# Performance work log

Hardware: AMD Instinct MI355X
Metric: run time of the kernel (lower is better)

The kernel has to match this reference:

```python
import jax, jax.numpy as jnp
import numpy as np

B, T, D, K = 32, 1024, 256, 1024


def setup_inputs() -> dict:
    key = jax.random.key(0)
    k1, k2 = jax.random.split(key)
    x = jax.random.normal(k1, (B, T, D), dtype=jnp.float32)
    # nn.Embedding init: uniform(-1/emb_size, 1/emb_size)
    embedding = jax.random.uniform(k2, (K, D), dtype=jnp.float32,
                                   minval=-1.0 / K, maxval=1.0 / K)
    return {"x": x, "embedding": embedding}


def reference(x, embedding):
    # x: [B, T, D], embedding: [K, D]
    Bx, Tx, Dx = x.shape
    flat = x.reshape(-1, Dx)  # [N, D]
    dist = (jnp.sum(embedding * embedding, axis=1)
            - 2.0 * flat @ embedding.T
            + jnp.sum(flat * flat, axis=1, keepdims=True))
    quantized_idx = jnp.argmin(dist, axis=1).reshape(Bx, Tx)  # [B, T] int
    # onehot @ W  ==  gather rows of W
    embed_idx = embedding[quantized_idx]  # [B, T, D]
    # straight-through estimator
    embed_idx_qx = x + jax.lax.stop_gradient(embed_idx - x)
    return embed_idx, embed_idx_qx, quantized_idx
```

## Files before the change

### kernel.cpp

```cpp
#include <hip/hip_runtime.h>
#include <math.h>

#define N_ROWS 32768
#define DIM    256
#define KCODES 1024
#define DELTA  1.5e-4f

typedef float f32x4 __attribute__((ext_vector_type(4)));
typedef short s16x8 __attribute__((ext_vector_type(8)));

__device__ inline unsigned short bf_rne(float f) {
    unsigned u = __float_as_uint(f);
    return (unsigned short)((u + 0x7FFFu + ((u >> 16) & 1u)) >> 16);
}
__device__ inline float bf_to_f(unsigned short h) {
    return __uint_as_float(((unsigned)h) << 16);
}

__device__ inline void ins4(float v, int ix, float (&tv)[4], int (&ti)[4]) {
    if (v < tv[3] || (v == tv[3] && ix < ti[3])) {
        if (v < tv[2] || (v == tv[2] && ix < ti[2])) {
            tv[3] = tv[2]; ti[3] = ti[2];
            if (v < tv[1] || (v == tv[1] && ix < ti[1])) {
                tv[2] = tv[1]; ti[2] = ti[1];
                if (v < tv[0] || (v == tv[0] && ix < ti[0])) {
                    tv[1] = tv[0]; ti[1] = ti[0]; tv[0] = v; ti[0] = ix;
                } else { tv[1] = v; ti[1] = ix; }
            } else { tv[2] = v; ti[2] = ix; }
        } else { tv[3] = v; ti[3] = ix; }
    }
}

__device__ __forceinline__ void gl_lds16(const void* gp, void* lp) {
    __builtin_amdgcn_global_load_lds(
        (__attribute__((address_space(1))) void*)(void*)gp,
        (__attribute__((address_space(3))) void*)lp, 16, 0, 0);
}

__global__ __launch_bounds__(256) void prep_kernel(const float* __restrict__ E,
                                                   const float* __restrict__ X,
                                                   float* __restrict__ e2,
                                                   float* __restrict__ x2,
                                                   unsigned short* __restrict__ Eh,
                                                   unsigned short* __restrict__ El) {
    __shared__ float sq[4][260];
    const int wave = threadIdx.x >> 6;
    const int lane = threadIdx.x & 63;
    if (blockIdx.x < KCODES / 4) {
        const int row = blockIdx.x * 4 + wave;
        const float4* rp = (const float4*)(E + (size_t)row * DIM);
        float4 v = rp[lane];
        sq[wave][lane * 4 + 0] = v.x * v.x;
        sq[wave][lane * 4 + 1] = v.y * v.y;
        sq[wave][lane * 4 + 2] = v.z * v.z;
        sq[wave][lane * 4 + 3] = v.w * v.w;
        float fs[4] = {v.x, v.y, v.z, v.w};
        ushort4 hv, lv;
        unsigned short* hp = (unsigned short*)&hv;
        unsigned short* lp = (unsigned short*)&lv;
#pragma unroll
        for (int j = 0; j < 4; ++j) {
            unsigned short h = bf_rne(fs[j]);
            hp[j] = h;
            lp[j] = bf_rne(fs[j] - bf_to_f(h));
        }
        *(ushort4*)(Eh + (size_t)row * DIM + lane * 4) = hv;
        *(ushort4*)(El + (size_t)row * DIM + lane * 4) = lv;
        if (lane < 8) {
#pragma clang fp contract(off)
            const int j = lane;
            float rA = sq[wave][j];
#pragma unroll
            for (int m = 1; m < 16; ++m) rA += sq[wave][8 * m + j];
            float rB = sq[wave][128 + j];
#pragma unroll
            for (int m = 1; m < 16; ++m) rB += sq[wave][128 + 8 * m + j];
            rA = rA + __shfl_xor(rA, 1, 64); rA = rA + __shfl_xor(rA, 2, 64);
            rA = rA + __shfl_xor(rA, 4, 64);
            rB = rB + __shfl_xor(rB, 1, 64); rB = rB + __shfl_xor(rB, 2, 64);
            rB = rB + __shfl_xor(rB, 4, 64);
            if (j == 0) e2[row] = rA + rB;
        }
    } else {
        const int row = (blockIdx.x - KCODES / 4) * 4 + wave;
        if (row >= N_ROWS) return;
        const float4* rp = (const float4*)(X + (size_t)row * DIM);
        float4 v = rp[lane];
        sq[wave][lane * 4 + 0] = v.x * v.x;
        sq[wave][lane * 4 + 1] = v.y * v.y;
        sq[wave][lane * 4 + 2] = v.z * v.z;
        sq[wave][lane * 4 + 3] = v.w * v.w;
        if (lane < 8) {
#pragma clang fp contract(off)
            const int j = lane;
            float rA = sq[wave][j];
#pragma unroll
            for (int m = 1; m < 16; ++m) rA += sq[wave][8 * m + j];
            float rB = sq[wave][128 + j];
#pragma unroll
            for (int m = 1; m < 16; ++m) rB += sq[wave][128 + 8 * m + j];
            rA = rA + __shfl_xor(rA, 1, 64); rA = rA + __shfl_xor(rA, 2, 64);
            rA = rA + __shfl_xor(rA, 4, 64);
            rB = rB + __shfl_xor(rB, 1, 64); rB = rB + __shfl_xor(rB, 2, 64);
            rB = rB + __shfl_xor(rB, 4, 64);
            if (j == 0) x2[row] = rA + rB;
        }
    }
}

__global__ __launch_bounds__(512, 2) void vq_mfma_kernel(const float* __restrict__ X,
                                                         const unsigned short* __restrict__ Eh,
                                                         const unsigned short* __restrict__ El,
                                                         const float* __restrict__ e2g,
                                                         float* __restrict__ topv,
                                                         int* __restrict__ topi) {
    __shared__ __align__(16) short bh_lds[2][16384];
    __shared__ __align__(16) short bl_lds[2][16384];
    __shared__ float e2_lds[KCODES];

    const int tid  = threadIdx.x;
    const int w    = tid >> 6;
    const int l    = tid & 63;
    const int c16  = l & 15;
    const int quad = l >> 4;
    const int p    = w & 3;
    const int grp  = w >> 2;
    const int row0 = blockIdx.x * 128;

    if (tid < 256) *(float4*)&e2_lds[tid * 4] = *(const float4*)&e2g[tid * 4];

    s16x8 xh[2][8], xl[2][8];
#pragma unroll
    for (int t = 0; t < 2; ++t) {
        const float* xrow = X + (size_t)(row0 + p * 32 + t * 16 + c16) * DIM + quad * 8;
#pragma unroll
        for (int ks = 0; ks < 8; ++ks) {
            float4 f0 = *(const float4*)(xrow + ks * 32);
            float4 f1 = *(const float4*)(xrow + ks * 32 + 4);
            float fs[8] = {f0.x, f0.y, f0.z, f0.w, f1.x, f1.y, f1.z, f1.w};
#pragma unroll
            for (int j = 0; j < 8; ++j) {
                unsigned short h = bf_rne(fs[j]);
                xh[t][ks][j] = (short)h;
                xl[t][ks][j] = (short)bf_rne(fs[j] - bf_to_f(h));
            }
        }
    }

    float tva[4], tvb[4];
    int   tia[4], tib[4];
#pragma unroll
    for (int s = 0; s < 4; ++s) {
        tva[s] = INFINITY; tvb[s] = INFINITY;
        tia[s] = 0x7fffffff; tib[s] = 0x7fffffff;
    }

    auto stage = [&](int bsel, int cb) {
#pragma unroll
        for (int gg = 0; gg < 4; ++gg) {
            const int g  = w + gg * 8;
            const int nt = g >> 3, ks = g & 7;
            const size_t eo = (size_t)(cb + nt * 16 + c16) * DIM + ks * 32 + quad * 8;
            gl_lds16(Eh + eo, &bh_lds[bsel][g * 512]);
            gl_lds16(El + eo, &bl_lds[bsel][g * 512]);
        }
    };

    stage(0, 0);

    for (int c = 0; c < 16; ++c) {
        __syncthreads();
        if (c < 15) stage((c + 1) & 1, (c + 1) * 64);
        const int bsel = c & 1;
#pragma unroll
        for (int ntt = 0; ntt < 2; ++ntt) {
            const int nt = grp * 2 + ntt;
            f32x4 c0a = {0.f, 0.f, 0.f, 0.f};
            f32x4 c1a = c0a, c2a = c0a, c0b = c0a, c1b = c0a, c2b = c0a;
#pragma unroll
            for (int ks = 0; ks < 8; ++ks) {
                const int off = ((nt * 8 + ks) * 64 + l) * 8;
                s16x8 ch = *(const s16x8*)&bh_lds[bsel][off];
                s16x8 cl = *(const s16x8*)&bl_lds[bsel][off];
                c0a = __builtin_amdgcn_mfma_f32_16x16x32_bf16(ch, xh[0][ks], c0a, 0, 0, 0);
                c0b = __builtin_amdgcn_mfma_f32_16x16x32_bf16(ch, xh[1][ks], c0b, 0, 0, 0);
                c1a = __builtin_amdgcn_mfma_f32_16x16x32_bf16(cl, xh[0][ks], c1a, 0, 0, 0);
                c1b = __builtin_amdgcn_mfma_f32_16x16x32_bf16(cl, xh[1][ks], c1b, 0, 0, 0);
                c2a = __builtin_amdgcn_mfma_f32_16x16x32_bf16(ch, xl[0][ks], c2a, 0, 0, 0);
                c2b = __builtin_amdgcn_mfma_f32_16x16x32_bf16(ch, xl[1][ks], c2b, 0, 0, 0);
            }
#pragma unroll
            for (int r = 0; r < 4; ++r) {
                const int code = c * 64 + nt * 16 + quad * 4 + r;
                const float e2v = e2_lds[code];
                float da = c0a[r] + c1a[r] + c2a[r];
                float db = c0b[r] + c1b[r] + c2b[r];
                ins4(e2v - 2.0f * da, code, tva, tia);
                ins4(e2v - 2.0f * db, code, tvb, tib);
            }
        }
    }

#pragma unroll
    for (int st = 16; st <= 32; st <<= 1) {
        float ov[4]; int oi[4];
#pragma unroll
        for (int s = 0; s < 4; ++s) {
            ov[s] = __shfl_xor(tva[s], st, 64);
            oi[s] = __shfl_xor(tia[s], st, 64);
        }
#pragma unroll
        for (int s = 0; s < 4; ++s) ins4(ov[s], oi[s], tva, tia);
#pragma unroll
        for (int s = 0; s < 4; ++s) {
            ov[s] = __shfl_xor(tvb[s], st, 64);
            oi[s] = __shfl_xor(tib[s], st, 64);
        }
#pragma unroll
        for (int s = 0; s < 4; ++s) ins4(ov[s], oi[s], tvb, tib);
    }

    float* mv = (float*)&bh_lds[0][0];
    int*   mi = (int*)&bh_lds[0][4096];
    if (grp == 1 && quad == 0) {
        const int sa = p * 32 + c16;
        const int sb = sa + 16;
#pragma unroll
        for (int s = 0; s < 4; ++s) {
            mv[sa * 4 + s] = tva[s]; mi[sa * 4 + s] = tia[s];
            mv[sb * 4 + s] = tvb[s]; mi[sb * 4 + s] = tib[s];
        }
    }
    __syncthreads();
    if (grp == 0 && quad == 0) {
        const int sa = p * 32 + c16;
        const int sb = sa + 16;
#pragma unroll
        for (int s = 0; s < 4; ++s) ins4(mv[sa * 4 + s], mi[sa * 4 + s], tva, tia);
#pragma unroll
        for (int s = 0; s < 4; ++s) ins4(mv[sb * 4 + s], mi[sb * 4 + s], tvb, tib);
        const int ga = row0 + p * 32 + c16;
        const int gb = ga + 16;
#pragma unroll
        for (int s = 0; s < 4; ++s) {
            topv[ga * 4 + s] = tva[s]; topi[ga * 4 + s] = tia[s];
            topv[gb * 4 + s] = tvb[s]; topi[gb * 4 + s] = tib[s];
        }
    }
}

__global__ __launch_bounds__(256) void decide_gather_kernel(const float* __restrict__ X,
                                                            const float* __restrict__ E,
                                                            const float* __restrict__ e2g,
                                                            const float* __restrict__ x2g,
                                                            const float* __restrict__ topv,
                                                            const int* __restrict__ topi,
                                                            float* __restrict__ out0,
                                                            float* __restrict__ out1,
                                                            float* __restrict__ out2) {
    __shared__ int sidx[64];
    const int tid  = threadIdx.x;
    const int row0 = blockIdx.x * 64;
    if (tid < 64) {
        const int r = row0 + tid;
        float tv[4]; int ti[4];
#pragma unroll
        for (int s = 0; s < 4; ++s) { tv[s] = topv[r * 4 + s]; ti[s] = topi[r * 4 + s]; }

        int best = ti[0];
        if (!(tv[1] > tv[0] + DELTA)) {
            const float* xr = X + (size_t)r * DIM;
            const float x2v = x2g[r];
            float bq = INFINITY; int bi = 0x7fffffff;
            for (int cnd = 0; cnd < 4; ++cnd) {
                if (tv[cnd] <= tv[0] + DELTA) {
                    const int k = ti[cnd];
                    const float* er = E + (size_t)k * DIM;
                    float dot = 0.f;
                    for (int d = 0; d < DIM; d += 4) {
                        float4 xv = *(const float4*)(xr + d);
                        float4 ev = *(const float4*)(er + d);
                        dot = fmaf(xv.x, ev.x, dot);
                        dot = fmaf(xv.y, ev.y, dot);
                        dot = fmaf(xv.z, ev.z, dot);
                        dot = fmaf(xv.w, ev.w, dot);
                    }
                    float t1 = e2g[k] - 2.0f * dot;
                    float q  = t1 + x2v;
                    if (q < bq || (q == bq && k < bi)) { bq = q; bi = k; }
                }
            }
            best = bi;
        }
        sidx[tid] = best;
        out2[r] = (float)best;
    }
    __syncthreads();
#pragma unroll
    for (int it = 0; it < 16; ++it) {
        int f = tid + it * 256;
        int rr = f >> 6;
        int pp = f & 63;
        int ix = sidx[rr];
        float4 v = *(const float4*)(E + (size_t)ix * DIM + pp * 4);
        size_t o = (size_t)(row0 + rr) * DIM + (size_t)pp * 4;
        *(float4*)(out0 + o) = v;
        *(float4*)(out1 + o) = v;
    }
}

extern "C" void kernel_launch(void* const* d_in, const int* in_sizes, int n_in,
                              void* d_out, int out_size, void* d_ws, size_t ws_size,
                              hipStream_t stream) {
    const float* X = (const float*)d_in[0];
    const float* E = (const float*)d_in[1];

    float* e2 = (float*)d_ws;
    float* x2 = e2 + KCODES;
    unsigned short* Eh = (unsigned short*)(x2 + N_ROWS);
    unsigned short* El = Eh + KCODES * DIM;
    float* topv = (float*)(El + KCODES * DIM);
    int*   topi = (int*)(topv + N_ROWS * 4);

    float* out0 = (float*)d_out;
    float* out1 = out0 + (size_t)N_ROWS * DIM;
    float* out2 = out1 + (size_t)N_ROWS * DIM;

    prep_kernel<<<dim3(KCODES / 4 + N_ROWS / 4), dim3(256), 0, stream>>>(E, X, e2, x2,
                                                                         Eh, El);
    vq_mfma_kernel<<<dim3(N_ROWS / 128), dim3(512), 0, stream>>>(X, Eh, El, e2,
                                                                 topv, topi);
    decide_gather_kernel<<<dim3(N_ROWS / 64), dim3(256), 0, stream>>>(X, E, e2, x2,
                                                                      topv, topi,
                                                                      out0, out1, out2);
}
```

Baseline: 233.3 us.

## Drop bf16 split-precision terms, fuse decide/gather into MFMA kernel, widen rescore margin

Replaces the three-term bf16x3 split-precision distance GEMM with a single bf16 product, which removes the low-part embedding buffer and two thirds of the MFMA work. To compensate, the rescore margin DELTA is widened, so more rows fall back to exact fp32 rescoring of their top-4 candidates. The separate decide/gather kernel is folded into the MFMA kernel, which now processes 64 rows per block with 4 waves per tile across codes and merges the top-4 lists in LDS. This removes the topv/topi round trip through global memory and one launch. The risk is that plain bf16 error exceeds the margin or that the true argmin falls outside the top-4, and the rescoring path runs on one lane per row, which serializes work.

```diff
diff --git a/kernel.cpp b/kernel.cpp
--- a/kernel.cpp
+++ b/kernel.cpp
@@ -4,7 +4,7 @@
 #define N_ROWS 32768
 #define DIM    256
 #define KCODES 1024
-#define DELTA  1.5e-4f
+#define DELTA  5.0e-4f
 
 typedef float f32x4 __attribute__((ext_vector_type(4)));
 typedef short s16x8 __attribute__((ext_vector_type(8)));
@@ -12,9 +12,6 @@
 __device__ inline unsigned short bf_rne(float f) {
     unsigned u = __float_as_uint(f);
     return (unsigned short)((u + 0x7FFFu + ((u >> 16) & 1u)) >> 16);
-}
-__device__ inline float bf_to_f(unsigned short h) {
-    return __uint_as_float(((unsigned)h) << 16);
 }
 
 __device__ inline void ins4(float v, int ix, float (&tv)[4], int (&ti)[4]) {
@@ -41,8 +38,7 @@
                                                    const float* __restrict__ X,
                                                    float* __restrict__ e2,
                                                    float* __restrict__ x2,
-                                                   unsigned short* __restrict__ Eh,
-                                                   unsigned short* __restrict__ El) {
+                                                   unsigned short* __restrict__ Eh) {
     __shared__ float sq[4][260];
     const int wave = threadIdx.x >> 6;
     const int lane = threadIdx.x & 63;
@@ -55,17 +51,11 @@
         sq[wave][lane * 4 + 2] = v.z * v.z;
         sq[wave][lane * 4 + 3] = v.w * v.w;
         float fs[4] = {v.x, v.y, v.z, v.w};
-        ushort4 hv, lv;
+        ushort4 hv;
         unsigned short* hp = (unsigned short*)&hv;
-        unsigned short* lp = (unsigned short*)&lv;
-#pragma unroll
-        for (int j = 0; j < 4; ++j) {
-            unsigned short h = bf_rne(fs[j]);
-            hp[j] = h;
-            lp[j] = bf_rne(fs[j] - bf_to_f(h));
-        }
+#pragma unroll
+        for (int j = 0; j < 4; ++j) hp[j] = bf_rne(fs[j]);
         *(ushort4*)(Eh + (size_t)row * DIM + lane * 4) = hv;
-        *(ushort4*)(El + (size_t)row * DIM + lane * 4) = lv;
         if (lane < 8) {
 #pragma clang fp contract(off)
             const int j = lane;
@@ -108,28 +98,30 @@
     }
 }
 
-__global__ __launch_bounds__(512, 2) void vq_mfma_kernel(const float* __restrict__ X,
-                                                         const unsigned short* __restrict__ Eh,
-                                                         const unsigned short* __restrict__ El,
-                                                         const float* __restrict__ e2g,
-                                                         float* __restrict__ topv,
-                                                         int* __restrict__ topi) {
+__global__ __launch_bounds__(512, 4) void vq_fused_kernel(const float* __restrict__ X,
+                                                          const unsigned short* __restrict__ Eh,
+                                                          const float* __restrict__ e2g,
+                                                          const float* __restrict__ x2g,
+                                                          const float* __restrict__ E,
+                                                          float* __restrict__ out0,
+                                                          float* __restrict__ out1,
+                                                          float* __restrict__ out2) {
     __shared__ __align__(16) short bh_lds[2][16384];
-    __shared__ __align__(16) short bl_lds[2][16384];
     __shared__ float e2_lds[KCODES];
+    __shared__ int sidx[64];
 
     const int tid  = threadIdx.x;
     const int w    = tid >> 6;
     const int l    = tid & 63;
     const int c16  = l & 15;
     const int quad = l >> 4;
-    const int p    = w & 3;
-    const int grp  = w >> 2;
-    const int row0 = blockIdx.x * 128;
+    const int p    = w & 1;
+    const int grp  = w >> 1;
+    const int row0 = blockIdx.x * 64;
 
     if (tid < 256) *(float4*)&e2_lds[tid * 4] = *(const float4*)&e2g[tid * 4];
 
-    s16x8 xh[2][8], xl[2][8];
+    s16x8 xh[2][8];
 #pragma unroll
     for (int t = 0; t < 2; ++t) {
         const float* xrow = X + (size_t)(row0 + p * 32 + t * 16 + c16) * DIM + quad * 8;
@@ -139,11 +131,7 @@
             float4 f1 = *(const float4*)(xrow + ks * 32 + 4);
             float fs[8] = {f0.x, f0.y, f0.z, f0.w, f1.x, f1.y, f1.z, f1.w};
 #pragma unroll
-            for (int j = 0; j < 8; ++j) {
-                unsigned short h = bf_rne(fs[j]);
-                xh[t][ks][j] = (short)h;
-                xl[t][ks][j] = (short)bf_rne(fs[j] - bf_to_f(h));
-            }
+            for (int j = 0; j < 8; ++j) xh[t][ks][j] = (short)bf_rne(fs[j]);
         }
     }
 
@@ -156,13 +144,13 @@
     }
 
     auto stage = [&](int bsel, int cb) {
+        const unsigned short* Ehc = Eh + (size_t)cb * DIM;
 #pragma unroll
         for (int gg = 0; gg < 4; ++gg) {
             const int g  = w + gg * 8;
             const int nt = g >> 3, ks = g & 7;
-            const size_t eo = (size_t)(cb + nt * 16 + c16) * DIM + ks * 32 + quad * 8;
-            gl_lds16(Eh + eo, &bh_lds[bsel][g * 512]);
-            gl_lds16(El + eo, &bl_lds[bsel][g * 512]);
+            const size_t eo = (size_t)(nt * 16 + c16) * DIM + ks * 32 + quad * 8;
+            gl_lds16(Ehc + eo, &bh_lds[bsel][g * 512]);
         }
     };
 
@@ -172,32 +160,21 @@
         __syncthreads();
         if (c < 15) stage((c + 1) & 1, (c + 1) * 64);
         const int bsel = c & 1;
-#pragma unroll
-        for (int ntt = 0; ntt < 2; ++ntt) {
-            const int nt = grp * 2 + ntt;
-            f32x4 c0a = {0.f, 0.f, 0.f, 0.f};
-            f32x4 c1a = c0a, c2a = c0a, c0b = c0a, c1b = c0a, c2b = c0a;
-#pragma unroll
-            for (int ks = 0; ks < 8; ++ks) {
-                const int off = ((nt * 8 + ks) * 64 + l) * 8;
-                s16x8 ch = *(const s16x8*)&bh_lds[bsel][off];
-                s16x8 cl = *(const s16x8*)&bl_lds[bsel][off];
-                c0a = __builtin_amdgcn_mfma_f32_16x16x32_bf16(ch, xh[0][ks], c0a, 0, 0, 0);
-                c0b = __builtin_amdgcn_mfma_f32_16x16x32_bf16(ch, xh[1][ks], c0b, 0, 0, 0);
-                c1a = __builtin_amdgcn_mfma_f32_16x16x32_bf16(cl, xh[0][ks], c1a, 0, 0, 0);
-                c1b = __builtin_amdgcn_mfma_f32_16x16x32_bf16(cl, xh[1][ks], c1b, 0, 0, 0);
-                c2a = __builtin_amdgcn_mfma_f32_16x16x32_bf16(ch, xl[0][ks], c2a, 0, 0, 0);
-                c2b = __builtin_amdgcn_mfma_f32_16x16x32_bf16(ch, xl[1][ks], c2b, 0, 0, 0);
-            }
-#pragma unroll
-            for (int r = 0; r < 4; ++r) {
-                const int code = c * 64 + nt * 16 + quad * 4 + r;
-                const float e2v = e2_lds[code];
-                float da = c0a[r] + c1a[r] + c2a[r];
-                float db = c0b[r] + c1b[r] + c2b[r];
-                ins4(e2v - 2.0f * da, code, tva, tia);
-                ins4(e2v - 2.0f * db, code, tvb, tib);
-            }
+        const int nt   = grp;
+        f32x4 c0a = {0.f, 0.f, 0.f, 0.f};
+        f32x4 c0b = c0a;
+#pragma unroll
+        for (int ks = 0; ks < 8; ++ks) {
+            s16x8 ch = *(const s16x8*)&bh_lds[bsel][((nt * 8 + ks) * 64 + l) * 8];
+            c0a = __builtin_amdgcn_mfma_f32_16x16x32_bf16(ch, xh[0][ks], c0a, 0, 0, 0);
+            c0b = __builtin_amdgcn_mfma_f32_16x16x32_bf16(ch, xh[1][ks], c0b, 0, 0, 0);
+        }
+        f32x4 e2v = *(const f32x4*)&e2_lds[c * 64 + nt * 16 + quad * 4];
+#pragma unroll
+        for (int r = 0; r < 4; ++r) {
+            const int code = c * 64 + nt * 16 + quad * 4 + r;
+            ins4(fmaf(-2.0f, c0a[r], e2v[r]), code, tva, tia);
+            ins4(fmaf(-2.0f, c0b[r], e2v[r]), code, tvb, tib);
         }
     }
 
@@ -221,9 +198,9 @@
     }
 
     float* mv = (float*)&bh_lds[0][0];
-    int*   mi = (int*)&bh_lds[0][4096];
-    if (grp == 1 && quad == 0) {
-        const int sa = p * 32 + c16;
+    int*   mi = (int*)&bh_lds[0][8192];
+    if (grp >= 1 && quad == 0) {
+        const int sa = (grp - 1) * 64 + p * 32 + c16;
         const int sb = sa + 16;
 #pragma unroll
         for (int s = 0; s < 4; ++s) {
@@ -233,72 +210,54 @@
     }
     __syncthreads();
     if (grp == 0 && quad == 0) {
-        const int sa = p * 32 + c16;
-        const int sb = sa + 16;
-#pragma unroll
-        for (int s = 0; s < 4; ++s) ins4(mv[sa * 4 + s], mi[sa * 4 + s], tva, tia);
-#pragma unroll
-        for (int s = 0; s < 4; ++s) ins4(mv[sb * 4 + s], mi[sb * 4 + s], tvb, tib);
-        const int ga = row0 + p * 32 + c16;
-        const int gb = ga + 16;
-#pragma unroll
-        for (int s = 0; s < 4; ++s) {
-            topv[ga * 4 + s] = tva[s]; topi[ga * 4 + s] = tia[s];
-            topv[gb * 4 + s] = tvb[s]; topi[gb * 4 + s] = tib[s];
-        }
-    }
-}
-
-__global__ __launch_bounds__(256) void decide_gather_kernel(const float* __restrict__ X,
-                                                            const float* __restrict__ E,
-                                                            const float* __restrict__ e2g,
-                                                            const float* __restrict__ x2g,
-                                                            const float* __restrict__ topv,
-                                                            const int* __restrict__ topi,
-                                                            float* __restrict__ out0,
-                                                            float* __restrict__ out1,
-                                                            float* __restrict__ out2) {
-    __shared__ int sidx[64];
-    const int tid  = threadIdx.x;
-    const int row0 = blockIdx.x * 64;
-    if (tid < 64) {
-        const int r = row0 + tid;
-        float tv[4]; int ti[4];
-#pragma unroll
-        for (int s = 0; s < 4; ++s) { tv[s] = topv[r * 4 + s]; ti[s] = topi[r * 4 + s]; }
-
-        int best = ti[0];
-        if (!(tv[1] > tv[0] + DELTA)) {
-            const float* xr = X + (size_t)r * DIM;
-            const float x2v = x2g[r];
-            float bq = INFINITY; int bi = 0x7fffffff;
-            for (int cnd = 0; cnd < 4; ++cnd) {
-                if (tv[cnd] <= tv[0] + DELTA) {
-                    const int k = ti[cnd];
-                    const float* er = E + (size_t)k * DIM;
-                    float dot = 0.f;
-                    for (int d = 0; d < DIM; d += 4) {
-                        float4 xv = *(const float4*)(xr + d);
-                        float4 ev = *(const float4*)(er + d);
-                        dot = fmaf(xv.x, ev.x, dot);
-                        dot = fmaf(xv.y, ev.y, dot);
-                        dot = fmaf(xv.z, ev.z, dot);
-                        dot = fmaf(xv.w, ev.w, dot);
+#pragma unroll
+        for (int g2 = 1; g2 < 4; ++g2) {
+            const int sa = (g2 - 1) * 64 + p * 32 + c16;
+            const int sb = sa + 16;
+#pragma unroll
+            for (int s = 0; s < 4; ++s) ins4(mv[sa * 4 + s], mi[sa * 4 + s], tva, tia);
+#pragma unroll
+            for (int s = 0; s < 4; ++s) ins4(mv[sb * 4 + s], mi[sb * 4 + s], tvb, tib);
+        }
+#pragma unroll
+        for (int t = 0; t < 2; ++t) {
+            float* tv = t ? tvb : tva;
+            int*   ti = t ? tib : tia;
+            const int r = row0 + p * 32 + t * 16 + c16;
+            int best = ti[0];
+            if (!(tv[1] > tv[0] + DELTA)) {
+                const float* xr = X + (size_t)r * DIM;
+                const float x2v = x2g[r];
+                float bq = INFINITY; int bi = 0x7fffffff;
+                for (int cnd = 0; cnd < 4; ++cnd) {
+                    if (tv[cnd] <= tv[0] + DELTA) {
+                        const int k = ti[cnd];
+                        const float* er = E + (size_t)k * DIM;
+                        float dot = 0.f;
+                        for (int d = 0; d < DIM; d += 4) {
+                            float4 xv = *(const float4*)(xr + d);
+                            float4 ev = *(const float4*)(er + d);
+                            dot = fmaf(xv.x, ev.x, dot);
+                            dot = fmaf(xv.y, ev.y, dot);
+                            dot = fmaf(xv.z, ev.z, dot);
+                            dot = fmaf(xv.w, ev.w, dot);
+                        }
+                        float t1 = e2_lds[k] - 2.0f * dot;
+                        float q  = t1 + x2v;
+                        if (q < bq || (q == bq && k < bi)) { bq = q; bi = k; }
                     }
-                    float t1 = e2g[k] - 2.0f * dot;
-                    float q  = t1 + x2v;
-                    if (q < bq || (q == bq && k < bi)) { bq = q; bi = k; }
                 }
+                best = bi;
             }
-            best = bi;
-        }
-        sidx[tid] = best;
-        out2[r] = (float)best;
+            sidx[p * 32 + t * 16 + c16] = best;
+            out2[r] = (float)best;
+        }
     }
     __syncthreads();
-#pragma unroll
-    for (int it = 0; it < 16; ++it) {
-        int f = tid + it * 256;
+
+#pragma unroll
+    for (int it = 0; it < 8; ++it) {
+        int f = tid + it * 512;
         int rr = f >> 6;
         int pp = f & 63;
         int ix = sidx[rr];
@@ -318,19 +277,12 @@
     float* e2 = (float*)d_ws;
     float* x2 = e2 + KCODES;
     unsigned short* Eh = (unsigned short*)(x2 + N_ROWS);
-    unsigned short* El = Eh + KCODES * DIM;
-    float* topv = (float*)(El + KCODES * DIM);
-    int*   topi = (int*)(topv + N_ROWS * 4);
 
     float* out0 = (float*)d_out;
     float* out1 = out0 + (size_t)N_ROWS * DIM;
     float* out2 = out1 + (size_t)N_ROWS * DIM;
 
-    prep_kernel<<<dim3(KCODES / 4 + N_ROWS / 4), dim3(256), 0, stream>>>(E, X, e2, x2,
-                                                                         Eh, El);
-    vq_mfma_kernel<<<dim3(N_ROWS / 128), dim3(512), 0, stream>>>(X, Eh, El, e2,
-                                                                 topv, topi);
-    decide_gather_kernel<<<dim3(N_ROWS / 64), dim3(256), 0, stream>>>(X, E, e2, x2,
-                                                                      topv, topi,
-                                                                      out0, out1, out2);
-}
+    prep_kernel<<<dim3(KCODES / 4 + N_ROWS / 4), dim3(256), 0, stream>>>(E, X, e2, x2, Eh);
+    vq_fused_kernel<<<dim3(N_ROWS / 64), dim3(512), 0, stream>>>(X, Eh, e2, x2, E,
+                                                                 out0, out1, out2);
+}
```

New measurement: 201.7 us. 13.5% less time.
